# Optimization experiments

Hardware: AMD Instinct MI355X
Metric: run time of the kernel (lower is better)

## Reference

```python
import jax, jax.numpy as jnp
import numpy as np

K, B, D, H, C, T = 3, 512, 1024, 512, 48, 25  # num_TAB, batch, linear_dim, hidden, n_classes, max_len

def setup_inputs() -> dict:
    key = jax.random.key(0)
    ks = jax.random.split(key, 18)
    rn = lambda k, s, sc=0.02: (jax.random.normal(k, s, jnp.float32) * sc)
    return {
        'S_ppps': jax.random.normal(ks[0], (K, B, D), jnp.float32),
        'R_ppps': jax.random.normal(ks[1], (K, B, D), jnp.float32),
        'cls_W': rn(ks[2], (K, 2 * D, C)), 'cls_b': jnp.zeros((K, C), jnp.float32),
        'dur_W': rn(ks[3], (K * D, 1)), 'dur_b': jnp.zeros((1,), jnp.float32),
        'lin_W': rn(ks[4], (2 * K * D + K * C, D + 1)), 'lin_b': jnp.zeros((D + 1,), jnp.float32),
        'W_ih': rn(ks[5], (4 * H, D + 1)), 'W_hh': rn(ks[6], (4 * H, H)),
        'b_ih': jnp.zeros((4 * H,), jnp.float32), 'b_hh': jnp.zeros((4 * H,), jnp.float32),
        'Wp': rn(ks[7], (H, C)), 'bp': jnp.zeros((C,), jnp.float32),
        'Wdur': rn(ks[8], (D + H, 1)), 'bdur': jnp.zeros((1,), jnp.float32),
        'embed': rn(ks[9], (C, D), 1.0),
        'Wattn': rn(ks[10], (H, D)),
    }

def reference(S_ppps, R_ppps, cls_W, cls_b, dur_W, dur_b, lin_W, lin_b,
              W_ih, W_hh, b_ih, b_hh, Wp, bp, Wdur, bdur, embed, Wattn):
    S_stack = jnp.transpose(S_ppps, (1, 0, 2))            # [B,K,D] (torch.stack(S_ppps,1))
    # per-TAB classifiers: Y[i] = softmax(Linear(cat(S_i,R_i)))
    SR = jnp.concatenate([S_ppps, R_ppps], axis=-1)       # [K,B,2D]
    Y = jax.nn.softmax(jnp.einsum('kbd,kdc->kbc', SR, cls_W) + cls_b[:, None, :], axis=-1)  # [K,B,C]
    Yf = jnp.transpose(Y, (1, 0, 2)).reshape(B, K * C)    # cat(Y0..Yk) feature-wise
    Sf = jnp.transpose(S_ppps, (1, 0, 2)).reshape(B, K * D)
    Rf = jnp.transpose(R_ppps, (1, 0, 2)).reshape(B, K * D)
    feat = jnp.concatenate([Yf, Sf, Rf], axis=1)          # [B, K*C + 2*K*D]
    x0 = feat @ lin_W + lin_b                             # [B, D+1]
    curr_dur = Rf @ dur_W + dur_b                         # [B,1]
    inv_sqrt_d = 1.0 / np.sqrt(D).astype(np.float32)

    def step(carry, _):
        x, h, c, prev_h = carry
        gates = x @ W_ih.T + b_ih + h @ W_hh.T + b_hh     # [B,4H], torch gate order i,f,g,o
        i_g, f_g, g_g, o_g = jnp.split(gates, 4, axis=1)
        c = jax.nn.sigmoid(f_g) * c + jax.nn.sigmoid(i_g) * jnp.tanh(g_g)
        h = jax.nn.sigmoid(o_g) * jnp.tanh(c)
        logits = h @ Wp + bp                              # [B,C]
        q = (h @ Wattn) * inv_sqrt_d                      # [B,D]
        aw = jax.nn.softmax(jnp.einsum('bd,bkd->bk', q, S_stack), axis=-1)
        att = jnp.einsum('bk,bkd->bd', aw, S_stack)       # [B,D]
        dur = jnp.concatenate([att, prev_h], axis=1) @ Wdur + bdur  # [B,1]
        labels = jnp.argmax(logits, axis=1)
        probs = jax.nn.softmax(logits, axis=1)
        nx = jnp.concatenate([embed[labels], dur], axis=1)  # [B,D+1]
        return (nx, h, c, h), (labels, probs, dur[:, 0], att)

    z = jnp.zeros((B, H), x0.dtype)
    _, (labels_t, probs_t, dur_t, att_t) = jax.lax.scan(step, (x0, z, z, z), None, length=T)
    curr_action = jnp.sum(Y, axis=0)                      # [B,C]
    pred_class_probs = jnp.transpose(probs_t, (1, 0, 2))  # [B,T,C]
    pred_action_durations = jnp.concatenate([curr_dur, dur_t.T], axis=1)  # [B,T+1]
    return (labels_t, pred_class_probs, curr_action, pred_action_durations, att_t)
```

## Files before the change

kernel.cpp:

```cpp
#include <hip/hip_runtime.h>
#include <math.h>

#define B 512
#define D 1024
#define H 512
#define C 48
#define K 3
#define T 25
#define DP1 1025
#define G4H 2048
#define NC 3120
#define KP 1056
#define FK 6304

typedef _Float16 f16;
typedef _Float16 half8 __attribute__((ext_vector_type(8)));
typedef float floatx4 __attribute__((ext_vector_type(4)));

__device__ __forceinline__ float sigf(float x){ return 1.0f/(1.0f+expf(-x)); }


template<int MODE>
__device__ __forceinline__ void mf_load(
    const f16* __restrict__ Ahi, const f16* __restrict__ Alo,
    const f16* __restrict__ Bhi, const f16* __restrict__ Blo,
    int M, int lda, int ldb, int m0, int n0, int kbase, int k0, int t,
    const f16* __restrict__ Yh, const f16* __restrict__ Yl,
    const float* __restrict__ Sf, const float* __restrict__ Rf,
    half8& rah, half8& ral, half8& rbh, half8& rbl)
{
    int r = t>>2, seg = t&3;
    int kk = k0 + seg*8;
    {
        size_t off = (size_t)(n0+r)*ldb + kbase + kk;
        rbh = *(const half8*)(Bhi + off);
        rbl = *(const half8*)(Blo + off);
    }
    int m = m0 + r;
    if (MODE==0){
        if (m < M){
            size_t off = (size_t)m*lda + kbase + kk;
            rah = *(const half8*)(Ahi + off);
            ral = *(const half8*)(Alo + off);
        } else {
            #pragma unroll
            for (int i=0;i<8;i++){ rah[i]=(f16)0; ral[i]=(f16)0; }
        }
    } else {
        int kabs = kbase + kk;
        if (kabs < 144){
            rah = *(const half8*)(Yh + (size_t)m*144 + kabs);
            ral = *(const half8*)(Yl + (size_t)m*144 + kabs);
        } else if (kabs < 6288){
            int kp = kabs - 144;
            const float* src = (kp < 3*D)
                ? (Sf + (size_t)(kp>>10)*(B*D) + (size_t)m*D + (kp&(D-1)))
                : (Rf + (size_t)((kp-3*D)>>10)*(B*D) + (size_t)m*D + ((kp-3*D)&(D-1)));
            float4 f0 = *(const float4*)src;
            float4 f1 = *(const float4*)(src+4);
            float fv[8]={f0.x,f0.y,f0.z,f0.w,f1.x,f1.y,f1.z,f1.w};
            #pragma unroll
            for (int i=0;i<8;i++){
                f16 h=(f16)fv[i];
                rah[i]=h; ral[i]=(f16)(fv[i]-(float)h);
            }
        } else {
            #pragma unroll
            for (int i=0;i<8;i++){ rah[i]=(f16)0; ral[i]=(f16)0; }
        }
    }
}

template<int MODE>
__global__ __launch_bounds__(256)
void k_mfma(const f16* __restrict__ Ahi, const f16* __restrict__ Alo,
            const f16* __restrict__ Bhi, const f16* __restrict__ Blo,
            float* __restrict__ Cc, const float* __restrict__ bias,
            int M, int Nvalid, int Ktot, int lda, int ldb, int ldc,
            int ksl, size_t cstride, int MB, int Z,
            const f16* __restrict__ Yh, const f16* __restrict__ Yl,
            const float* __restrict__ Sf, const float* __restrict__ Rf)
{
    __shared__ __align__(16) f16 Ash[2][64][40];
    __shared__ __align__(16) f16 Asl[2][64][40];
    __shared__ __align__(16) f16 Bsh[2][64][40];
    __shared__ __align__(16) f16 Bsl[2][64][40];
    int t = threadIdx.x;
    int chunk = gridDim.x >> 3;
    int g = (blockIdx.x & 7)*chunk + (blockIdx.x >> 3);
    int mz   = g % (MB*Z);
    int nblk = g / (MB*Z);
    int mblk = mz / Z;
    int z    = mz % Z;
    int m0 = mblk*64, n0 = nblk*64;
    int kbase = z*ksl;
    int kcnt = (z==Z-1)? (Ktot-kbase) : ksl;
    int nIter = kcnt >> 5;
    int r = t>>2, seg = t&3;
    half8 rah, ral, rbh, rbl;
    mf_load<MODE>(Ahi,Alo,Bhi,Blo,M,lda,ldb,m0,n0,kbase,0,t,Yh,Yl,Sf,Rf,rah,ral,rbh,rbl);
    int lane = t&63, wv = t>>6;
    int lrow = lane&15, quad = lane>>4;
    floatx4 acc[4] = {};
    int cur = 0;
    for (int it=0; it<nIter; ++it){
        *(half8*)&Ash[cur][r][seg*8] = rah;
        *(half8*)&Asl[cur][r][seg*8] = ral;
        *(half8*)&Bsh[cur][r][seg*8] = rbh;
        *(half8*)&Bsl[cur][r][seg*8] = rbl;
        if (it+1 < nIter)
            mf_load<MODE>(Ahi,Alo,Bhi,Blo,M,lda,ldb,m0,n0,kbase,(it+1)<<5,t,Yh,Yl,Sf,Rf,rah,ral,rbh,rbl);
        __syncthreads();
        half8 ah = *(const half8*)&Ash[cur][wv*16+lrow][quad*8];
        half8 al = *(const half8*)&Asl[cur][wv*16+lrow][quad*8];
        #pragma unroll
        for (int j=0;j<4;j++){
            half8 bh = *(const half8*)&Bsh[cur][j*16+lrow][quad*8];
            half8 bl = *(const half8*)&Bsl[cur][j*16+lrow][quad*8];
            acc[j] = __builtin_amdgcn_mfma_f32_16x16x32_f16(ah, bh, acc[j], 0,0,0);
            acc[j] = __builtin_amdgcn_mfma_f32_16x16x32_f16(al, bh, acc[j], 0,0,0);
            acc[j] = __builtin_amdgcn_mfma_f32_16x16x32_f16(ah, bl, acc[j], 0,0,0);
        }
        cur ^= 1;
    }
    float* Cz = Cc + (size_t)z*cstride;
    #pragma unroll
    for (int j=0;j<4;j++){
        int col = n0 + j*16 + lrow;
        if (col >= Nvalid) continue;
        float bv = bias ? bias[col] : 0.f;
        #pragma unroll
        for (int i=0;i<4;i++){
            int row = m0 + wv*16 + quad*4 + i;
            if (row < M) Cz[(size_t)row*ldc + col] = acc[j][i] + bv;
        }
    }
}


__global__ void k_bt_build(const float* __restrict__ src, f16* __restrict__ hi, f16* __restrict__ lo,
                           int Ksrc, int Nsrc, int ld_src, int NB, int KB, float scale){
    __shared__ float tile[32][33];
    int k0 = blockIdx.x*32, n0 = blockIdx.y*32;
    int lx = threadIdx.x & 31, ly = threadIdx.x >> 5;
    for (int rr=0; rr<32; rr+=8){
        int k2 = k0+ly+rr, n = n0+lx;
        tile[ly+rr][lx] = (k2<Ksrc && n<Nsrc)? src[(size_t)k2*ld_src+n]*scale : 0.f;
    }
    __syncthreads();
    for (int rr=0; rr<32; rr+=8){
        int n = n0+ly+rr, k2 = k0+lx;
        if (n<NB && k2<KB){
            float v = tile[lx][ly+rr];
            f16 h=(f16)v;
            hi[(size_t)n*KB+k2]=h;
            lo[(size_t)n*KB+k2]=(f16)(v-(float)h);
        }
    }
}

__global__ void k_permrows(const float* __restrict__ src, f16* __restrict__ hi, f16* __restrict__ lo,
                           int src_ld, int dst_ld, int kvalid){
    int idx = blockIdx.x*256+threadIdx.x;
    if (idx >= G4H*dst_ld) return;
    int p = idx/dst_ld, k2 = idx%dst_ld;
    int j = p>>2, g = p&3, gi = (g<<9)|j;
    float v = (k2<kvalid)? src[(size_t)gi*src_ld + k2] : 0.f;
    f16 h=(f16)v;
    hi[idx]=h; lo[idx]=(f16)(v-(float)h);
}

__global__ void k_cvt(const float* __restrict__ src, f16* __restrict__ hi, f16* __restrict__ lo,
                      int M, int ld_src, int nvalid, int ld_dst){
    int idx = blockIdx.x*256+threadIdx.x;
    if (idx >= M*ld_dst) return;
    int m = idx/ld_dst, n = idx%ld_dst;
    float v = (n<nvalid)? src[(size_t)m*ld_src+n] : 0.f;
    f16 h=(f16)v; hi[idx]=h; lo[idx]=(f16)(v-(float)h);
}

__global__ void k_cvtY(const float* __restrict__ Y, f16* __restrict__ hi, f16* __restrict__ lo){
    int idx = blockIdx.x*256+threadIdx.x;
    if (idx >= B*144) return;
    int b = idx/144, k2 = idx%144;
    float v = Y[((size_t)(k2/C)*B + b)*C + (k2%C)];
    f16 h=(f16)v; hi[idx]=h; lo[idx]=(f16)(v-(float)h);
}

__global__ void k_zeroh(f16* a, f16* b2, int n){
    int i = blockIdx.x*256+threadIdx.x; if (i<n){ a[i]=(f16)0; b2[i]=(f16)0; }
}

__global__ void k_prep(const float* __restrict__ bih, const float* __restrict__ bhh,
                       const float* __restrict__ bp, const float* __restrict__ Wih,
                       float* __restrict__ bias2p, float* __restrict__ biascat,
                       float* __restrict__ wl){
    int i = blockIdx.x*256 + threadIdx.x;
    if (i < G4H){
        int g=i&3, j=i>>2; int gi=(g<<9)|j;
        bias2p[i]=bih[gi]+bhh[gi];
        wl[i]=Wih[(size_t)gi*DP1 + 1024];
    }
    if (i < C) biascat[i]=bp[i];
}

__global__ void k_cls(const float* __restrict__ S, const float* __restrict__ R,
                      const float* __restrict__ clsW, const float* __restrict__ clsb,
                      float* __restrict__ Y){
    int kb = blockIdx.x; int k = kb / B; int b = kb % B;
    int t = threadIdx.x;
    __shared__ float sr[64];
    __shared__ float lg[C];
    __shared__ float mred[2];
    float acc = (t<C) ? clsb[k*C+t] : 0.f;
    const float* W = clsW + (size_t)k*2*D*C;
    for (int i0=0; i0<2*D; i0+=64){
        int i = i0 + t;
        sr[t] = (i < D) ? S[((size_t)k*B+b)*D + i] : R[((size_t)k*B+b)*D + (i-D)];
        __syncthreads();
        if (t < C){ for (int ii=0; ii<64; ++ii) acc += sr[ii]*W[(size_t)(i0+ii)*C + t]; }
        __syncthreads();
    }
    if (t<C) lg[t]=acc;
    __syncthreads();
    if (t==0){
        float m=lg[0]; for(int c2=1;c2<C;c2++) m=fmaxf(m,lg[c2]);
        float s=0.f; for(int c2=0;c2<C;c2++) s+=expf(lg[c2]-m);
        mred[0]=m; mred[1]=s;
    }
    __syncthreads();
    if (t<C) Y[((size_t)k*B+b)*C + t] = expf(lg[t]-mred[0])/mred[1];
}

__global__ void k_curr_action(const float* __restrict__ Y, float* __restrict__ outca){
    int i = blockIdx.x*256+threadIdx.x; if (i>=B*C) return;
    int b=i/C, c2=i%C;
    outca[i] = Y[((size_t)0*B+b)*C+c2] + Y[((size_t)1*B+b)*C+c2] + Y[((size_t)2*B+b)*C+c2];
}

__global__ void k_dur0(const float* __restrict__ R, const float* __restrict__ durW,
                       const float* __restrict__ durb, float* __restrict__ outpad){
    int b = blockIdx.x; int t = threadIdx.x;
    __shared__ float red[256];
    float p=0.f;
    for (int i=t; i<K*D; i+=256){ int k=i>>10, d=i&1023; p += R[((size_t)k*B+b)*D+d]*durW[i]; }
    red[t]=p; __syncthreads();
    for (int s=128;s>0;s>>=1){ if(t<s) red[t]+=red[t+s]; __syncthreads(); }
    if (t==0) outpad[(size_t)b*(T+1)] = red[0] + durb[0];
}

__global__ void k_red(float* __restrict__ dst, const float* __restrict__ src, int parts, size_t pstride,
                      int M, int Nld, int Nvalid, const float* __restrict__ bias){
    int idx = blockIdx.x*256+threadIdx.x;
    if (idx >= M*Nld) return;
    int n = idx % Nld;
    float v = 0.f;
    if (n < Nvalid){
        for (int p=0;p<parts;p++) v += src[(size_t)p*pstride + idx];
        if (bias) v += bias[n];
    }
    dst[idx]=v;
}

__global__ void k_redcvt(const float* __restrict__ src, int parts, size_t pstride,
                         const float* __restrict__ bias, f16* __restrict__ hi, f16* __restrict__ lo){
    int idx = blockIdx.x*256+threadIdx.x;
    if (idx >= 512*KP) return;
    int m = idx/KP, n = idx%KP;
    float v = 0.f;
    if (n < DP1){
        for (int p=0;p<parts;p++) v += src[(size_t)p*pstride + (size_t)m*1028 + n];
        v += bias[n];
    }
    f16 h=(f16)v; hi[idx]=h; lo[idx]=(f16)(v-(float)h);
}


__global__ void k_lstm0(const float* __restrict__ gxp, int parts, size_t pstride,
                        const float* __restrict__ bias2p,
                        float* __restrict__ c, f16* __restrict__ hhi, f16* __restrict__ hlo){
    int idx = blockIdx.x*256+threadIdx.x; if (idx>=B*H) return;
    int r=idx>>9, j=idx&511;
    float4 g = *(const float4*)&gxp[(size_t)r*G4H + (j<<2)];
    if (parts==2){
        float4 g2 = *(const float4*)&gxp[pstride + (size_t)r*G4H + (j<<2)];
        g.x+=g2.x; g.y+=g2.y; g.z+=g2.z; g.w+=g2.w;
    }
    float4 bb = *(const float4*)&bias2p[j<<2];
    g.x+=bb.x; g.y+=bb.y; g.z+=bb.z; g.w+=bb.w;
    float cn = sigf(g.x)*tanhf(g.z);
    c[idx]=cn;
    float hv = sigf(g.w)*tanhf(cn);
    f16 h=(f16)hv; hhi[idx]=h; hlo[idx]=(f16)(hv-(float)h);
}

__global__ void k_postapply(const float* __restrict__ rawg, int parts, size_t pstride,
                       const float* __restrict__ S,
                       const f16* __restrict__ holdhi, const f16* __restrict__ holdlo,
                       const float* __restrict__ E, const float* __restrict__ wl,
                       const float* __restrict__ biascat,
                       const float* __restrict__ Wdur, const float* __restrict__ bdur,
                       float* __restrict__ outlab, float* __restrict__ outprobs,
                       float* __restrict__ outatt, float* __restrict__ outpad,
                       int* __restrict__ labs, float* __restrict__ wsdur,
                       float* __restrict__ c, f16* __restrict__ hNhi, f16* __restrict__ hNlo,
                       int tstep, int doLstm)
{
    int b=blockIdx.x, t=threadIdx.x;
    int lane=t&63, wv=t>>6;
    __shared__ float lg[C];
    __shared__ float aw[3];
    __shared__ float redw[4][8];
    __shared__ int sbest;
    __shared__ float sdv;
    const float* z0 = rawg + (size_t)b*NC;
    const float* z1 = z0 + pstride;
    if (t<C){
        float v = z0[G4H+t]; if (parts==2) v += z1[G4H+t];
        lg[t] = v + biascat[t];
    }
    if (t<64){
        float m = (t<C)? lg[t] : -1e30f;
        int bi = t;
        #pragma unroll
        for (int s=32;s>0;s>>=1){
            float om=__shfl_down(m,s); int ob=__shfl_down(bi,s);
            if (om>m || (om==m && ob<bi)){ m=om; bi=ob; }
        }
        m=__shfl(m,0); bi=__shfl(bi,0);
        float e=(t<C)? expf(lg[t]-m):0.f;
        float ss=e;
        #pragma unroll
        for (int s=32;s>0;s>>=1) ss+=__shfl_down(ss,s);
        ss=__shfl(ss,0);
        if (t==0){
            labs[b]=bi; sbest=bi;
            outlab[(size_t)tstep*B+b]=(float)bi;
        }
        if (t<C) outprobs[(size_t)b*(T*C)+tstep*C+t]=expf(lg[t]-m)/ss;
    }
    const float* S0 = S + (size_t)b*D;
    const float* S1 = S0 + (size_t)B*D;
    const float* S2 = S1 + (size_t)B*D;
    const float* q0 = z0 + G4H + C;
    const float* q1 = z1 + G4H + C;
    float pv0=0.f,pv1=0.f,pv2=0.f;
    for (int d=t; d<D; d+=512){
        float qd=q0[d]; if (parts==2) qd+=q1[d];
        pv0+=qd*S0[d]; pv1+=qd*S1[d]; pv2+=qd*S2[d];
    }
    #pragma unroll
    for (int s=32;s>0;s>>=1){
        pv0+=__shfl_down(pv0,s); pv1+=__shfl_down(pv1,s); pv2+=__shfl_down(pv2,s);
    }
    if (lane==0){ redw[0][wv]=pv0; redw[1][wv]=pv1; redw[2][wv]=pv2; }
    __syncthreads();
    if (t==0){
        float a0=0.f,a1=0.f,a2=0.f;
        #pragma unroll
        for (int w=0;w<8;w++){ a0+=redw[0][w]; a1+=redw[1][w]; a2+=redw[2][w]; }
        float m=fmaxf(a0,fmaxf(a1,a2));
        float e0=expf(a0-m), e1=expf(a1-m), e2=expf(a2-m);
        float si=1.f/(e0+e1+e2);
        aw[0]=e0*si; aw[1]=e1*si; aw[2]=e2*si;
    }
    __syncthreads();
    float a0=aw[0],a1=aw[1],a2=aw[2];
    float dp=0.f;
    for (int d=t; d<D; d+=512){
        float av=a0*S0[d]+a1*S1[d]+a2*S2[d];
        outatt[(size_t)tstep*B*D + (size_t)b*D + d]=av;
        dp+=av*Wdur[d];
    }
    if (holdhi){
        for (int p=t;p<H;p+=512)
            dp += ((float)holdhi[(size_t)b*H+p] + (float)holdlo[(size_t)b*H+p])*Wdur[D+p];
    }
    #pragma unroll
    for (int s=32;s>0;s>>=1) dp+=__shfl_down(dp,s);
    if (lane==0) redw[3][wv]=dp;
    __syncthreads();
    if (t==0){
        float dv=0.f;
        #pragma unroll
        for (int w=0;w<8;w++) dv+=redw[3][w];
        dv += bdur[0];
        outpad[(size_t)b*(T+1)+tstep+1]=dv; wsdur[b]=dv; sdv=dv;
    }
    __syncthreads();
    if (doLstm){
        int lb=sbest; float dv=sdv;
        int j=t;
        float4 g4 = *(const float4*)&z0[4*j];
        if (parts==2){
            float4 h4 = *(const float4*)&z1[4*j];
            g4.x+=h4.x; g4.y+=h4.y; g4.z+=h4.z; g4.w+=h4.w;
        }
        float4 e4 = *(const float4*)&E[(size_t)lb*G4H+4*j];
        float4 w4 = *(const float4*)&wl[4*j];
        float gi=g4.x+e4.x+dv*w4.x;
        float gf=g4.y+e4.y+dv*w4.y;
        float gg=g4.z+e4.z+dv*w4.z;
        float go=g4.w+e4.w+dv*w4.w;
        size_t ci=(size_t)b*H+j;
        float cn = sigf(gf)*c[ci] + sigf(gi)*tanhf(gg);
        c[ci]=cn;
        float hv = sigf(go)*tanhf(cn);
        f16 hh=(f16)hv;
        hNhi[ci]=hh; hNlo[ci]=(f16)(hv-(float)hh);
    }
}


extern "C" void kernel_launch(void* const* d_in, const int* in_sizes, int n_in,
                              void* d_out, int out_size, void* d_ws, size_t ws_size,
                              hipStream_t stream) {
    const float* S    = (const float*)d_in[0];
    const float* R    = (const float*)d_in[1];
    const float* clsW = (const float*)d_in[2];
    const float* clsb = (const float*)d_in[3];
    const float* durW = (const float*)d_in[4];
    const float* durb = (const float*)d_in[5];
    const float* linW = (const float*)d_in[6];
    const float* linb = (const float*)d_in[7];
    const float* Wih  = (const float*)d_in[8];
    const float* Whh  = (const float*)d_in[9];
    const float* bih  = (const float*)d_in[10];
    const float* bhh  = (const float*)d_in[11];
    const float* Wp   = (const float*)d_in[12];
    const float* bp   = (const float*)d_in[13];
    const float* Wdur = (const float*)d_in[14];
    const float* bdur = (const float*)d_in[15];
    const float* embed= (const float*)d_in[16];
    const float* Wattn= (const float*)d_in[17];

    float* out = (float*)d_out;
    float* outlab   = out;
    float* outprobs = out + 12800;
    float* outca    = out + 627200;
    float* outpad   = out + 651776;
    float* outatt   = out + 665088;

    float* ws = (float*)d_ws;
    float* E       = ws + 0;
    float* wl      = ws + 98304;
    float* bias2p  = ws + 100352;
    float* biascat = ws + 102400;
    float* c       = ws + 102464;
    f16*   hAhi    = (f16*)(ws + 364608);
    f16*   hAlo    = (f16*)(ws + 495680);
    f16*   hBhi    = (f16*)(ws + 626752);
    f16*   hBlo    = (f16*)(ws + 757824);
    float* wsdur   = ws + 888896;
    int*   labs    = (int*)(ws + 889408);
    f16*   Yhi     = (f16*)(ws + 889920);
    f16*   Ylo     = (f16*)(ws + 926784);
    float* Y       = ws + 963648;
    f16*   x0hi    = (f16*)(ws + 1563712);
    f16*   x0lo    = (f16*)(ws + 1834048);
    f16*   embhi   = (f16*)(ws + 2104384);
    f16*   emblo   = (f16*)(ws + 2129728);
    const size_t SB = 2155072;
    f16*   lwthi   = (f16*)(ws + SB);
    f16*   lwtlo   = (f16*)(ws + SB + 3429376);
    float* x0part  = ws + SB + 6858752;
    f16*   Wcthi   = (f16*)(ws + SB);
    f16*   Wctlo   = (f16*)(ws + SB + 802816);
    f16*   Wihphi  = (f16*)(ws + SB + 1605632);
    f16*   Wihplo  = (f16*)(ws + SB + 2686976);
    float* rawg    = ws + SB + 4816896;
    float* gpart   = rawg;

    int ZX0, ksl_x0;
    if      (ws_size >= (size_t)52898048){ ZX0=8; ksl_x0=800;  }
    else if (ws_size >= (size_t)44476672){ ZX0=4; ksl_x0=1600; }
    else                                 { ZX0=2; ksl_x0=3168; }
    int ZSC    = (ws_size >= (size_t)40667392) ? 2 : 1;
    int ksl_sc = (ZSC==2) ? 256 : 512;
    const int ZGX = 2, ksl_gx = 544;
    const int ZE  = 4, ksl_e  = 256;

    k_prep<<<8,256,0,stream>>>(bih,bhh,bp,Wih,bias2p,biascat,wl);
    k_cls<<<K*B,64,0,stream>>>(S,R,clsW,clsb,Y);
    k_curr_action<<<(B*C+255)/256,256,0,stream>>>(Y,outca);
    k_cvtY<<<(B*144+255)/256,256,0,stream>>>(Y,Yhi,Ylo);
    k_dur0<<<B,256,0,stream>>>(R,durW,durb,outpad);
    k_bt_build<<<dim3((FK+31)/32,(1088+31)/32),256,0,stream>>>(linW,lwthi,lwtlo,6288,1025,1025,1088,FK,1.f);
    k_mfma<1><<<8*17*ZX0,256,0,stream>>>(nullptr,nullptr,lwthi,lwtlo,x0part,nullptr,
                                         512,1028,FK,0,FK,1028,ksl_x0,(size_t)512*1028,8,ZX0,
                                         Yhi,Ylo,S,R);
    k_redcvt<<<(512*KP+255)/256,256,0,stream>>>(x0part,ZX0,(size_t)512*1028,linb,x0hi,x0lo);
    k_permrows<<<(G4H*KP+255)/256,256,0,stream>>>(Wih,Wihphi,Wihplo,DP1,KP,DP1);
    k_mfma<0><<<8*32*ZGX,256,0,stream>>>(x0hi,x0lo,Wihphi,Wihplo,gpart,nullptr,
                                         512,G4H,KP,KP,KP,G4H,ksl_gx,(size_t)512*G4H,8,ZGX,
                                         nullptr,nullptr,nullptr,nullptr);
    k_lstm0<<<(B*H+255)/256,256,0,stream>>>(gpart,ZGX,(size_t)512*G4H,bias2p,c,hAhi,hAlo);
    k_cvt<<<(48*KP+255)/256,256,0,stream>>>(embed,embhi,emblo,48,1024,1024,KP);
    k_mfma<0><<<1*32*ZE,256,0,stream>>>(embhi,emblo,Wihphi,Wihplo,gpart,nullptr,
                                        48,G4H,KP,KP,KP,G4H,ksl_e,(size_t)48*G4H,1,ZE,
                                        nullptr,nullptr,nullptr,nullptr);
    k_red<<<(48*G4H+255)/256,256,0,stream>>>(E,gpart,ZE,(size_t)48*G4H,48,G4H,G4H,bias2p);
    k_permrows<<<(G4H*512+255)/256,256,0,stream>>>(Whh,Wcthi,Wctlo,H,H,H);
    k_bt_build<<<dim3(16,2),256,0,stream>>>(Wp,Wcthi+(size_t)2048*512,Wctlo+(size_t)2048*512,
                                            512,48,48,48,512,1.f);
    k_bt_build<<<dim3(16,32),256,0,stream>>>(Wattn,Wcthi+(size_t)2096*512,Wctlo+(size_t)2096*512,
                                             512,1024,1024,1024,512,0.03125f);
    k_zeroh<<<32,256,0,stream>>>(Wcthi+(size_t)3120*512,Wctlo+(size_t)3120*512,16*512);

    size_t pstr = (size_t)512*NC;
    f16 *hCurHi=hAhi, *hCurLo=hAlo, *hPrvHi=hBhi, *hPrvLo=hBlo;
    for (int t=0;t<T;t++){
        k_mfma<0><<<8*49*ZSC,256,0,stream>>>(hCurHi,hCurLo,Wcthi,Wctlo,rawg,nullptr,
                                             512,NC,H,H,H,NC,ksl_sc,pstr,8,ZSC,
                                             nullptr,nullptr,nullptr,nullptr);
        k_postapply<<<B,512,0,stream>>>(rawg,ZSC,pstr,S,(t==0)?nullptr:hPrvHi,(t==0)?nullptr:hPrvLo,
                                        E,wl,biascat,Wdur,bdur,
                                        outlab,outprobs,outatt,outpad,labs,wsdur,
                                        c,hPrvHi,hPrvLo,t,(t<T-1)?1:0);
        f16* th=hPrvHi; hPrvHi=hCurHi; hCurHi=th;
        f16* tl=hPrvLo; hPrvLo=hCurLo; hCurLo=tl;
    }
}
```

Baseline: 972.0 us.

## Fuse LSTM scan into persistent kernel with grid-wide atomic barriers

Replaces the per-timestep pair of GEMM and postprocessing launches with a single persistent kernel that loops over all timesteps and synchronises blocks through an atomic counter barrier. The recurrent weight high-part tile is kept resident in LDS, and cell and previous hidden state stay in registers. Each wave handles one batch row in the postprocessing phase. This removes launch overhead and split-K partial buffers, but relies on all 196 blocks being co-resident and adds spin-barrier cost per step.

```diff
diff --git a/kernel.cpp b/kernel.cpp
--- a/kernel.cpp
+++ b/kernel.cpp
@@ -12,6 +12,7 @@
 #define NC 3120
 #define KP 1056
 #define FK 6304
+#define NBLK 196
 
 typedef _Float16 f16;
 typedef _Float16 half8 __attribute__((ext_vector_type(8)));
@@ -194,8 +195,9 @@
 __global__ void k_prep(const float* __restrict__ bih, const float* __restrict__ bhh,
                        const float* __restrict__ bp, const float* __restrict__ Wih,
                        float* __restrict__ bias2p, float* __restrict__ biascat,
-                       float* __restrict__ wl){
+                       float* __restrict__ wl, unsigned* __restrict__ bar){
     int i = blockIdx.x*256 + threadIdx.x;
+    if (i == 0) *bar = 0u;
     if (i < G4H){
         int g=i&3, j=i>>2; int gi=(g<<9)|j;
         bias2p[i]=bih[gi]+bhh[gi];
@@ -275,7 +277,6 @@
     f16 h=(f16)v; hi[idx]=h; lo[idx]=(f16)(v-(float)h);
 }
 
-
 __global__ void k_lstm0(const float* __restrict__ gxp, int parts, size_t pstride,
                         const float* __restrict__ bias2p,
                         float* __restrict__ c, f16* __restrict__ hhi, f16* __restrict__ hlo){
@@ -294,120 +295,222 @@
     f16 h=(f16)hv; hhi[idx]=h; hlo[idx]=(f16)(hv-(float)h);
 }
 
-__global__ void k_postapply(const float* __restrict__ rawg, int parts, size_t pstride,
-                       const float* __restrict__ S,
-                       const f16* __restrict__ holdhi, const f16* __restrict__ holdlo,
-                       const float* __restrict__ E, const float* __restrict__ wl,
-                       const float* __restrict__ biascat,
-                       const float* __restrict__ Wdur, const float* __restrict__ bdur,
-                       float* __restrict__ outlab, float* __restrict__ outprobs,
-                       float* __restrict__ outatt, float* __restrict__ outpad,
-                       int* __restrict__ labs, float* __restrict__ wsdur,
-                       float* __restrict__ c, f16* __restrict__ hNhi, f16* __restrict__ hNlo,
-                       int tstep, int doLstm)
+__global__ __launch_bounds__(256,1)
+void k_scan(const f16* __restrict__ Bh_g, const f16* __restrict__ Bl_g,
+            f16* __restrict__ ghhi, f16* __restrict__ ghlo,
+            const float* __restrict__ cinit,
+            float* __restrict__ rawg,
+            const float* __restrict__ S,
+            const float* __restrict__ E, const float* __restrict__ wl,
+            const float* __restrict__ biascat,
+            const float* __restrict__ Wdur, const float* __restrict__ bdur,
+            float* __restrict__ outlab, float* __restrict__ outprobs,
+            float* __restrict__ outatt, float* __restrict__ outpad,
+            unsigned* __restrict__ bar)
 {
-    int b=blockIdx.x, t=threadIdx.x;
-    int lane=t&63, wv=t>>6;
-    __shared__ float lg[C];
-    __shared__ float aw[3];
-    __shared__ float redw[4][8];
-    __shared__ int sbest;
-    __shared__ float sdv;
-    const float* z0 = rawg + (size_t)b*NC;
-    const float* z1 = z0 + pstride;
-    if (t<C){
-        float v = z0[G4H+t]; if (parts==2) v += z1[G4H+t];
-        lg[t] = v + biascat[t];
-    }
-    if (t<64){
-        float m = (t<C)? lg[t] : -1e30f;
-        int bi = t;
+    __shared__ __align__(16) f16 Bsh[64][520];
+    __shared__ __align__(16) f16 Ash[2][128][40];
+    __shared__ __align__(16) f16 Asl[2][128][40];
+    const int t = threadIdx.x;
+    const int g = blockIdx.x;
+    const int lane = t & 63, wv = t >> 6;
+    const int lrow = lane & 15, quad = lane >> 4;
+    const int mblk = g & 3, nblk = g >> 2;
+    const int m0 = mblk << 7, n0 = nblk << 6;
+
+    for (int q = t; q < 64*64; q += 256){
+        int col = q >> 6, seg = q & 63;
+        *(half8*)&Bsh[col][seg<<3] = *(const half8*)(Bh_g + (size_t)(n0+col)*H + (seg<<3));
+    }
+
+    const int brow = g + NBLK*wv;
+    const bool act = brow < B;
+    float c_reg[8], hold_reg[8], hcur_reg[8];
+    if (act){
         #pragma unroll
-        for (int s=32;s>0;s>>=1){
-            float om=__shfl_down(m,s); int ob=__shfl_down(bi,s);
-            if (om>m || (om==m && ob<bi)){ m=om; bi=ob; }
-        }
-        m=__shfl(m,0); bi=__shfl(bi,0);
-        float e=(t<C)? expf(lg[t]-m):0.f;
-        float ss=e;
+        for (int i=0;i<8;i++){
+            int j = lane + (i<<6);
+            c_reg[i]   = cinit[(size_t)brow*H + j];
+            hold_reg[i]= 0.f;
+            hcur_reg[i]= (float)ghhi[(size_t)brow*H + j] + (float)ghlo[(size_t)brow*H + j];
+        }
+    }
+    const float bd0 = bdur[0];
+    unsigned gp = 0;
+    __syncthreads();
+
+    for (int ts=0; ts<T; ++ts){
+        floatx4 acc[2][4] = {};
+        half8 pa0h,pa0l,pa1h,pa1l;
+        {
+            int r0 = t>>2, s0 = (t&3)<<3;
+            size_t o0 = (size_t)(m0+r0)*H + s0;
+            size_t o1 = (size_t)(m0+64+r0)*H + s0;
+            pa0h = *(const half8*)(ghhi+o0); pa0l = *(const half8*)(ghlo+o0);
+            pa1h = *(const half8*)(ghhi+o1); pa1l = *(const half8*)(ghlo+o1);
+        }
+        half8 bl[2][4];
         #pragma unroll
-        for (int s=32;s>0;s>>=1) ss+=__shfl_down(ss,s);
-        ss=__shfl(ss,0);
+        for (int j=0;j<4;j++)
+            bl[0][j] = *(const half8*)(Bl_g + (size_t)(n0+j*16+lrow)*H + (quad<<3));
+        #pragma unroll 4
+        for (int it=0; it<16; ++it){
+            const int cur = it & 1;
+            *(half8*)&Ash[cur][t>>2][(t&3)<<3]        = pa0h;
+            *(half8*)&Asl[cur][t>>2][(t&3)<<3]        = pa0l;
+            *(half8*)&Ash[cur][64+(t>>2)][(t&3)<<3]   = pa1h;
+            *(half8*)&Asl[cur][64+(t>>2)][(t&3)<<3]   = pa1l;
+            if (it+1<16){
+                int r0 = t>>2, s0 = (t&3)<<3;
+                size_t o0 = (size_t)(m0+r0)*H + (it+1)*32 + s0;
+                size_t o1 = (size_t)(m0+64+r0)*H + (it+1)*32 + s0;
+                pa0h = *(const half8*)(ghhi+o0); pa0l = *(const half8*)(ghlo+o0);
+                pa1h = *(const half8*)(ghhi+o1); pa1l = *(const half8*)(ghlo+o1);
+            }
+            asm volatile("s_waitcnt lgkmcnt(0)" ::: "memory");
+            __builtin_amdgcn_s_barrier();
+            if (it+1<16){
+                #pragma unroll
+                for (int j=0;j<4;j++)
+                    bl[(it+1)&1][j] = *(const half8*)(Bl_g + (size_t)(n0+j*16+lrow)*H + (it+1)*32 + (quad<<3));
+            }
+            half8 ah0 = *(const half8*)&Ash[cur][(wv<<5)+lrow][quad<<3];
+            half8 al0 = *(const half8*)&Asl[cur][(wv<<5)+lrow][quad<<3];
+            half8 ah1 = *(const half8*)&Ash[cur][(wv<<5)+16+lrow][quad<<3];
+            half8 al1 = *(const half8*)&Asl[cur][(wv<<5)+16+lrow][quad<<3];
+            #pragma unroll
+            for (int j=0;j<4;j++){
+                half8 bh  = *(const half8*)&Bsh[j*16+lrow][(it<<5)+(quad<<3)];
+                half8 blj = bl[cur][j];
+                acc[0][j] = __builtin_amdgcn_mfma_f32_16x16x32_f16(ah0,bh, acc[0][j],0,0,0);
+                acc[0][j] = __builtin_amdgcn_mfma_f32_16x16x32_f16(al0,bh, acc[0][j],0,0,0);
+                acc[0][j] = __builtin_amdgcn_mfma_f32_16x16x32_f16(ah0,blj,acc[0][j],0,0,0);
+                acc[1][j] = __builtin_amdgcn_mfma_f32_16x16x32_f16(ah1,bh, acc[1][j],0,0,0);
+                acc[1][j] = __builtin_amdgcn_mfma_f32_16x16x32_f16(al1,bh, acc[1][j],0,0,0);
+                acc[1][j] = __builtin_amdgcn_mfma_f32_16x16x32_f16(ah1,blj,acc[1][j],0,0,0);
+            }
+        }
+        #pragma unroll
+        for (int j=0;j<4;j++){
+            int col = n0 + j*16 + lrow;
+            if (col < NC){
+                #pragma unroll
+                for (int rt=0;rt<2;rt++){
+                    int rbase = m0 + (wv<<5) + rt*16 + (quad<<2);
+                    #pragma unroll
+                    for (int i=0;i<4;i++)
+                        rawg[(size_t)(rbase+i)*NC + col] = acc[rt][j][i];
+                }
+            }
+        }
+        ++gp;
+        __syncthreads();
         if (t==0){
-            labs[b]=bi; sbest=bi;
-            outlab[(size_t)tstep*B+b]=(float)bi;
-        }
-        if (t<C) outprobs[(size_t)b*(T*C)+tstep*C+t]=expf(lg[t]-m)/ss;
-    }
-    const float* S0 = S + (size_t)b*D;
-    const float* S1 = S0 + (size_t)B*D;
-    const float* S2 = S1 + (size_t)B*D;
-    const float* q0 = z0 + G4H + C;
-    const float* q1 = z1 + G4H + C;
-    float pv0=0.f,pv1=0.f,pv2=0.f;
-    for (int d=t; d<D; d+=512){
-        float qd=q0[d]; if (parts==2) qd+=q1[d];
-        pv0+=qd*S0[d]; pv1+=qd*S1[d]; pv2+=qd*S2[d];
-    }
-    #pragma unroll
-    for (int s=32;s>0;s>>=1){
-        pv0+=__shfl_down(pv0,s); pv1+=__shfl_down(pv1,s); pv2+=__shfl_down(pv2,s);
-    }
-    if (lane==0){ redw[0][wv]=pv0; redw[1][wv]=pv1; redw[2][wv]=pv2; }
-    __syncthreads();
-    if (t==0){
-        float a0=0.f,a1=0.f,a2=0.f;
-        #pragma unroll
-        for (int w=0;w<8;w++){ a0+=redw[0][w]; a1+=redw[1][w]; a2+=redw[2][w]; }
-        float m=fmaxf(a0,fmaxf(a1,a2));
-        float e0=expf(a0-m), e1=expf(a1-m), e2=expf(a2-m);
-        float si=1.f/(e0+e1+e2);
-        aw[0]=e0*si; aw[1]=e1*si; aw[2]=e2*si;
-    }
-    __syncthreads();
-    float a0=aw[0],a1=aw[1],a2=aw[2];
-    float dp=0.f;
-    for (int d=t; d<D; d+=512){
-        float av=a0*S0[d]+a1*S1[d]+a2*S2[d];
-        outatt[(size_t)tstep*B*D + (size_t)b*D + d]=av;
-        dp+=av*Wdur[d];
-    }
-    if (holdhi){
-        for (int p=t;p<H;p+=512)
-            dp += ((float)holdhi[(size_t)b*H+p] + (float)holdlo[(size_t)b*H+p])*Wdur[D+p];
-    }
-    #pragma unroll
-    for (int s=32;s>0;s>>=1) dp+=__shfl_down(dp,s);
-    if (lane==0) redw[3][wv]=dp;
-    __syncthreads();
-    if (t==0){
-        float dv=0.f;
-        #pragma unroll
-        for (int w=0;w<8;w++) dv+=redw[3][w];
-        dv += bdur[0];
-        outpad[(size_t)b*(T+1)+tstep+1]=dv; wsdur[b]=dv; sdv=dv;
-    }
-    __syncthreads();
-    if (doLstm){
-        int lb=sbest; float dv=sdv;
-        int j=t;
-        float4 g4 = *(const float4*)&z0[4*j];
-        if (parts==2){
-            float4 h4 = *(const float4*)&z1[4*j];
-            g4.x+=h4.x; g4.y+=h4.y; g4.z+=h4.z; g4.w+=h4.w;
-        }
-        float4 e4 = *(const float4*)&E[(size_t)lb*G4H+4*j];
-        float4 w4 = *(const float4*)&wl[4*j];
-        float gi=g4.x+e4.x+dv*w4.x;
-        float gf=g4.y+e4.y+dv*w4.y;
-        float gg=g4.z+e4.z+dv*w4.z;
-        float go=g4.w+e4.w+dv*w4.w;
-        size_t ci=(size_t)b*H+j;
-        float cn = sigf(gf)*c[ci] + sigf(gi)*tanhf(gg);
-        c[ci]=cn;
-        float hv = sigf(go)*tanhf(cn);
-        f16 hh=(f16)hv;
-        hNhi[ci]=hh; hNlo[ci]=(f16)(hv-(float)hh);
+            __threadfence();
+            __hip_atomic_fetch_add(bar, 1u, __ATOMIC_RELEASE, __HIP_MEMORY_SCOPE_AGENT);
+            while (__hip_atomic_load(bar, __ATOMIC_ACQUIRE, __HIP_MEMORY_SCOPE_AGENT) < gp*NBLK)
+                __builtin_amdgcn_s_sleep(1);
+            __threadfence();
+        }
+        __syncthreads();
+
+        if (act){
+            const float* z0 = rawg + (size_t)brow*NC;
+            float lgv = (lane<C)? (z0[G4H+lane] + biascat[lane]) : -3.0e38f;
+            float mx = lgv; int bi = lane;
+            #pragma unroll
+            for (int s2=32;s2>0;s2>>=1){
+                float om = __shfl_xor(mx, s2); int ob = __shfl_xor(bi, s2);
+                if (om>mx || (om==mx && ob<bi)){ mx=om; bi=ob; }
+            }
+            float ev = (lane<C)? expf(lgv-mx) : 0.f;
+            float ss = ev;
+            #pragma unroll
+            for (int s2=32;s2>0;s2>>=1) ss += __shfl_xor(ss, s2);
+            if (lane<C) outprobs[(size_t)brow*(T*C) + ts*C + lane] = ev/ss;
+            if (lane==0) outlab[(size_t)ts*B + brow] = (float)bi;
+            const float* S0  = S + (size_t)brow*D;
+            const float* S1  = S0 + (size_t)B*D;
+            const float* S2p = S1 + (size_t)B*D;
+            const float* q   = z0 + G4H + C;
+            float p0=0.f,p1=0.f,p2=0.f;
+            #pragma unroll
+            for (int i=0;i<4;i++){
+                int d = ((i<<6)+lane)<<2;
+                float4 qv = *(const float4*)(q+d);
+                float4 s0 = *(const float4*)(S0+d);
+                float4 s1 = *(const float4*)(S1+d);
+                float4 s2 = *(const float4*)(S2p+d);
+                p0 += qv.x*s0.x+qv.y*s0.y+qv.z*s0.z+qv.w*s0.w;
+                p1 += qv.x*s1.x+qv.y*s1.y+qv.z*s1.z+qv.w*s1.w;
+                p2 += qv.x*s2.x+qv.y*s2.y+qv.z*s2.z+qv.w*s2.w;
+            }
+            #pragma unroll
+            for (int s2=32;s2>0;s2>>=1){
+                p0 += __shfl_xor(p0,s2); p1 += __shfl_xor(p1,s2); p2 += __shfl_xor(p2,s2);
+            }
+            float mm = fmaxf(p0,fmaxf(p1,p2));
+            float e0 = expf(p0-mm), e1 = expf(p1-mm), e2 = expf(p2-mm);
+            float inv = 1.f/(e0+e1+e2);
+            float a0=e0*inv, a1=e1*inv, a2=e2*inv;
+            float dp = 0.f;
+            float* attp = outatt + (size_t)ts*B*D + (size_t)brow*D;
+            #pragma unroll
+            for (int i=0;i<4;i++){
+                int d = ((i<<6)+lane)<<2;
+                float4 s0 = *(const float4*)(S0+d);
+                float4 s1 = *(const float4*)(S1+d);
+                float4 s2 = *(const float4*)(S2p+d);
+                float4 w4 = *(const float4*)(Wdur+d);
+                float4 av;
+                av.x = a0*s0.x+a1*s1.x+a2*s2.x;
+                av.y = a0*s0.y+a1*s1.y+a2*s2.y;
+                av.z = a0*s0.z+a1*s1.z+a2*s2.z;
+                av.w = a0*s0.w+a1*s1.w+a2*s2.w;
+                *(float4*)(attp+d) = av;
+                dp += av.x*w4.x+av.y*w4.y+av.z*w4.z+av.w*w4.w;
+            }
+            #pragma unroll
+            for (int i=0;i<8;i++) dp += hold_reg[i]*Wdur[D + lane + (i<<6)];
+            #pragma unroll
+            for (int s2=32;s2>0;s2>>=1) dp += __shfl_xor(dp,s2);
+            float dv = dp + bd0;
+            if (lane==0) outpad[(size_t)brow*(T+1) + ts + 1] = dv;
+            if (ts < T-1){
+                const float* Erow = E + (size_t)bi*G4H;
+                #pragma unroll
+                for (int i=0;i<8;i++){
+                    int j = lane + (i<<6);
+                    float4 g4 = *(const float4*)(z0 + (j<<2));
+                    float4 e4 = *(const float4*)(Erow + (j<<2));
+                    float4 w4 = *(const float4*)(wl + (j<<2));
+                    float gi = g4.x+e4.x+dv*w4.x;
+                    float gf = g4.y+e4.y+dv*w4.y;
+                    float gg = g4.z+e4.z+dv*w4.z;
+                    float go = g4.w+e4.w+dv*w4.w;
+                    float cn = sigf(gf)*c_reg[i] + sigf(gi)*tanhf(gg);
+                    c_reg[i] = cn;
+                    float hv = sigf(go)*tanhf(cn);
+                    f16 hh = (f16)hv;
+                    ghhi[(size_t)brow*H + j] = hh;
+                    ghlo[(size_t)brow*H + j] = (f16)(hv-(float)hh);
+                    hold_reg[i] = hcur_reg[i];
+                    hcur_reg[i] = hv;
+                }
+            }
+        }
+        if (ts+1 < T){
+            ++gp;
+            __syncthreads();
+            if (t==0){
+                __threadfence();
+                __hip_atomic_fetch_add(bar, 1u, __ATOMIC_RELEASE, __HIP_MEMORY_SCOPE_AGENT);
+                while (__hip_atomic_load(bar, __ATOMIC_ACQUIRE, __HIP_MEMORY_SCOPE_AGENT) < gp*NBLK)
+                    __builtin_amdgcn_s_sleep(1);
+                __threadfence();
+            }
+            __syncthreads();
+        }
     }
 }
 
@@ -449,10 +552,7 @@
     float* c       = ws + 102464;
     f16*   hAhi    = (f16*)(ws + 364608);
     f16*   hAlo    = (f16*)(ws + 495680);
-    f16*   hBhi    = (f16*)(ws + 626752);
-    f16*   hBlo    = (f16*)(ws + 757824);
-    float* wsdur   = ws + 888896;
-    int*   labs    = (int*)(ws + 889408);
+    unsigned* bar  = (unsigned*)(ws + 889408);
     f16*   Yhi     = (f16*)(ws + 889920);
     f16*   Ylo     = (f16*)(ws + 926784);
     float* Y       = ws + 963648;
@@ -475,12 +575,10 @@
     if      (ws_size >= (size_t)52898048){ ZX0=8; ksl_x0=800;  }
     else if (ws_size >= (size_t)44476672){ ZX0=4; ksl_x0=1600; }
     else                                 { ZX0=2; ksl_x0=3168; }
-    int ZSC    = (ws_size >= (size_t)40667392) ? 2 : 1;
-    int ksl_sc = (ZSC==2) ? 256 : 512;
     const int ZGX = 2, ksl_gx = 544;
     const int ZE  = 4, ksl_e  = 256;
 
-    k_prep<<<8,256,0,stream>>>(bih,bhh,bp,Wih,bias2p,biascat,wl);
+    k_prep<<<8,256,0,stream>>>(bih,bhh,bp,Wih,bias2p,biascat,wl,bar);
     k_cls<<<K*B,64,0,stream>>>(S,R,clsW,clsb,Y);
     k_curr_action<<<(B*C+255)/256,256,0,stream>>>(Y,outca);
     k_cvtY<<<(B*144+255)/256,256,0,stream>>>(Y,Yhi,Ylo);
@@ -507,17 +605,6 @@
                                              512,1024,1024,1024,512,0.03125f);
     k_zeroh<<<32,256,0,stream>>>(Wcthi+(size_t)3120*512,Wctlo+(size_t)3120*512,16*512);
 
-    size_t pstr = (size_t)512*NC;
-    f16 *hCurHi=hAhi, *hCurLo=hAlo, *hPrvHi=hBhi, *hPrvLo=hBlo;
-    for (int t=0;t<T;t++){
-        k_mfma<0><<<8*49*ZSC,256,0,stream>>>(hCurHi,hCurLo,Wcthi,Wctlo,rawg,nullptr,
-                                             512,NC,H,H,H,NC,ksl_sc,pstr,8,ZSC,
-                                             nullptr,nullptr,nullptr,nullptr);
-        k_postapply<<<B,512,0,stream>>>(rawg,ZSC,pstr,S,(t==0)?nullptr:hPrvHi,(t==0)?nullptr:hPrvLo,
-                                        E,wl,biascat,Wdur,bdur,
-                                        outlab,outprobs,outatt,outpad,labs,wsdur,
-                                        c,hPrvHi,hPrvLo,t,(t<T-1)?1:0);
-        f16* th=hPrvHi; hPrvHi=hCurHi; hCurHi=th;
-        f16* tl=hPrvLo; hPrvLo=hCurLo; hCurLo=tl;
-    }
-}
+    k_scan<<<NBLK,256,0,stream>>>(Wcthi,Wctlo,hAhi,hAlo,c,rawg,S,E,wl,biascat,Wdur,bdur,
+                                  outlab,outprobs,outatt,outpad,bar);
+}
```

Result: slower. 2.044 ms (+110.3%).

## Precompute S·Wattnᵀ so attention scores use hidden state directly

Applied to the files above, without the earlier changes.

Uses associativity: q·S_k = h·(Wattn·S_kᵀ), so V = S·Wattnᵀ (scaled) is computed once before the loop with an MFMA GEMM. The per-step GEMM then drops the 1024 attention-query columns (NC from 3120 to 2112), and the attention scores become a 512-wide dot of h with V inside the post kernel. The post kernel is also tidied with xor-shuffles, vectorized float2 loads, and unused label and duration workspace writes removed. The trade-off is an extra setup GEMM plus conversions and a change in rounding order for the scores.

```diff
diff --git a/kernel.cpp b/kernel.cpp
--- a/kernel.cpp
+++ b/kernel.cpp
@@ -9,7 +9,8 @@
 #define T 25
 #define DP1 1025
 #define G4H 2048
-#define NC 3120
+#define NC 2112
+#define NCV 2096
 #define KP 1056
 #define FK 6304
 
@@ -77,7 +78,7 @@
             const f16* __restrict__ Bhi, const f16* __restrict__ Blo,
             float* __restrict__ Cc, const float* __restrict__ bias,
             int M, int Nvalid, int Ktot, int lda, int ldb, int ldc,
-            int ksl, size_t cstride, int MB, int Z,
+            int ksl, size_t cstride, int MB, int Z, int zmaj,
             const f16* __restrict__ Yh, const f16* __restrict__ Yl,
             const float* __restrict__ Sf, const float* __restrict__ Rf)
 {
@@ -86,12 +87,19 @@
     __shared__ __align__(16) f16 Bsh[2][64][40];
     __shared__ __align__(16) f16 Bsl[2][64][40];
     int t = threadIdx.x;
-    int chunk = gridDim.x >> 3;
-    int g = (blockIdx.x & 7)*chunk + (blockIdx.x >> 3);
-    int mz   = g % (MB*Z);
-    int nblk = g / (MB*Z);
-    int mblk = mz / Z;
-    int z    = mz % Z;
+    int mblk, nblk, z;
+    if (zmaj){
+        z = blockIdx.x % Z;
+        int rest = blockIdx.x / Z;
+        mblk = rest % MB; nblk = rest / MB;
+    } else {
+        int chunk = gridDim.x >> 3;
+        int g = (blockIdx.x & 7)*chunk + (blockIdx.x >> 3);
+        int mz = g % (MB*Z);
+        nblk = g / (MB*Z);
+        mblk = mz / Z;
+        z    = mz % Z;
+    }
     int m0 = mblk*64, n0 = nblk*64;
     int kbase = z*ksl;
     int kcnt = (z==Z-1)? (Ktot-kbase) : ksl;
@@ -171,11 +179,11 @@
 }
 
 __global__ void k_cvt(const float* __restrict__ src, f16* __restrict__ hi, f16* __restrict__ lo,
-                      int M, int ld_src, int nvalid, int ld_dst){
+                      int M, int ld_src, int nvalid, int ld_dst, float scale){
     int idx = blockIdx.x*256+threadIdx.x;
     if (idx >= M*ld_dst) return;
     int m = idx/ld_dst, n = idx%ld_dst;
-    float v = (n<nvalid)? src[(size_t)m*ld_src+n] : 0.f;
+    float v = (n<nvalid)? src[(size_t)m*ld_src+n]*scale : 0.f;
     f16 h=(f16)v; hi[idx]=h; lo[idx]=(f16)(v-(float)h);
 }
 
@@ -295,65 +303,56 @@
 }
 
 __global__ void k_postapply(const float* __restrict__ rawg, int parts, size_t pstride,
-                       const float* __restrict__ S,
+                       const float* __restrict__ S, const float* __restrict__ V,
+                       const f16* __restrict__ hchi, const f16* __restrict__ hclo,
                        const f16* __restrict__ holdhi, const f16* __restrict__ holdlo,
                        const float* __restrict__ E, const float* __restrict__ wl,
                        const float* __restrict__ biascat,
                        const float* __restrict__ Wdur, const float* __restrict__ bdur,
                        float* __restrict__ outlab, float* __restrict__ outprobs,
                        float* __restrict__ outatt, float* __restrict__ outpad,
-                       int* __restrict__ labs, float* __restrict__ wsdur,
                        float* __restrict__ c, f16* __restrict__ hNhi, f16* __restrict__ hNlo,
                        int tstep, int doLstm)
 {
     int b=blockIdx.x, t=threadIdx.x;
     int lane=t&63, wv=t>>6;
-    __shared__ float lg[C];
     __shared__ float aw[3];
     __shared__ float redw[4][8];
     __shared__ int sbest;
     __shared__ float sdv;
     const float* z0 = rawg + (size_t)b*NC;
     const float* z1 = z0 + pstride;
-    if (t<C){
-        float v = z0[G4H+t]; if (parts==2) v += z1[G4H+t];
-        lg[t] = v + biascat[t];
-    }
     if (t<64){
-        float m = (t<C)? lg[t] : -1e30f;
-        int bi = t;
+        float lgv = -3.0e38f;
+        if (t<C){
+            float v = z0[G4H+t]; if (parts==2) v += z1[G4H+t];
+            lgv = v + biascat[t];
+        }
+        float m = lgv; int bi = t;
         #pragma unroll
-        for (int s=32;s>0;s>>=1){
-            float om=__shfl_down(m,s); int ob=__shfl_down(bi,s);
+        for (int s2=32;s2>0;s2>>=1){
+            float om=__shfl_xor(m,s2); int ob=__shfl_xor(bi,s2);
             if (om>m || (om==m && ob<bi)){ m=om; bi=ob; }
         }
-        m=__shfl(m,0); bi=__shfl(bi,0);
-        float e=(t<C)? expf(lg[t]-m):0.f;
+        float e=(t<C)? expf(lgv-m):0.f;
         float ss=e;
         #pragma unroll
-        for (int s=32;s>0;s>>=1) ss+=__shfl_down(ss,s);
-        ss=__shfl(ss,0);
+        for (int s2=32;s2>0;s2>>=1) ss+=__shfl_xor(ss,s2);
+        if (t<C) outprobs[(size_t)b*(T*C)+tstep*C+t]=e/ss;
         if (t==0){
-            labs[b]=bi; sbest=bi;
+            sbest=bi;
             outlab[(size_t)tstep*B+b]=(float)bi;
         }
-        if (t<C) outprobs[(size_t)b*(T*C)+tstep*C+t]=expf(lg[t]-m)/ss;
-    }
-    const float* S0 = S + (size_t)b*D;
-    const float* S1 = S0 + (size_t)B*D;
-    const float* S2 = S1 + (size_t)B*D;
-    const float* q0 = z0 + G4H + C;
-    const float* q1 = z1 + G4H + C;
-    float pv0=0.f,pv1=0.f,pv2=0.f;
-    for (int d=t; d<D; d+=512){
-        float qd=q0[d]; if (parts==2) qd+=q1[d];
-        pv0+=qd*S0[d]; pv1+=qd*S1[d]; pv2+=qd*S2[d];
-    }
+    }
+    float hv_t = (float)hchi[(size_t)b*H + t] + (float)hclo[(size_t)b*H + t];
+    float p0 = hv_t * V[((size_t)(0*B+b))*H + t];
+    float p1 = hv_t * V[((size_t)(1*B+b))*H + t];
+    float p2 = hv_t * V[((size_t)(2*B+b))*H + t];
     #pragma unroll
-    for (int s=32;s>0;s>>=1){
-        pv0+=__shfl_down(pv0,s); pv1+=__shfl_down(pv1,s); pv2+=__shfl_down(pv2,s);
-    }
-    if (lane==0){ redw[0][wv]=pv0; redw[1][wv]=pv1; redw[2][wv]=pv2; }
+    for (int s2=32;s2>0;s2>>=1){
+        p0 += __shfl_xor(p0,s2); p1 += __shfl_xor(p1,s2); p2 += __shfl_xor(p2,s2);
+    }
+    if (lane==0){ redw[0][wv]=p0; redw[1][wv]=p1; redw[2][wv]=p2; }
     __syncthreads();
     if (t==0){
         float a0=0.f,a1=0.f,a2=0.f;
@@ -366,18 +365,29 @@
     }
     __syncthreads();
     float a0=aw[0],a1=aw[1],a2=aw[2];
-    float dp=0.f;
-    for (int d=t; d<D; d+=512){
-        float av=a0*S0[d]+a1*S1[d]+a2*S2[d];
-        outatt[(size_t)tstep*B*D + (size_t)b*D + d]=av;
-        dp+=av*Wdur[d];
+    const float* S0  = S + (size_t)b*D;
+    const float* S1  = S0 + (size_t)B*D;
+    const float* S2p = S1 + (size_t)B*D;
+    float dp = 0.f;
+    float* attp = outatt + (size_t)tstep*B*D + (size_t)b*D;
+    {
+        int d = t<<1;
+        float2 s0 = *(const float2*)(S0+d);
+        float2 s1 = *(const float2*)(S1+d);
+        float2 s2 = *(const float2*)(S2p+d);
+        float2 w2 = *(const float2*)(Wdur+d);
+        float2 av;
+        av.x = a0*s0.x+a1*s1.x+a2*s2.x;
+        av.y = a0*s0.y+a1*s1.y+a2*s2.y;
+        *(float2*)(attp+d) = av;
+        dp += av.x*w2.x+av.y*w2.y;
     }
     if (holdhi){
-        for (int p=t;p<H;p+=512)
-            dp += ((float)holdhi[(size_t)b*H+p] + (float)holdlo[(size_t)b*H+p])*Wdur[D+p];
+        float hvo = (float)holdhi[(size_t)b*H+t] + (float)holdlo[(size_t)b*H+t];
+        dp += hvo * Wdur[D+t];
     }
     #pragma unroll
-    for (int s=32;s>0;s>>=1) dp+=__shfl_down(dp,s);
+    for (int s2=32;s2>0;s2>>=1) dp += __shfl_xor(dp,s2);
     if (lane==0) redw[3][wv]=dp;
     __syncthreads();
     if (t==0){
@@ -385,7 +395,7 @@
         #pragma unroll
         for (int w=0;w<8;w++) dv+=redw[3][w];
         dv += bdur[0];
-        outpad[(size_t)b*(T+1)+tstep+1]=dv; wsdur[b]=dv; sdv=dv;
+        outpad[(size_t)b*(T+1)+tstep+1]=dv; sdv=dv;
     }
     __syncthreads();
     if (doLstm){
@@ -398,10 +408,10 @@
         }
         float4 e4 = *(const float4*)&E[(size_t)lb*G4H+4*j];
         float4 w4 = *(const float4*)&wl[4*j];
-        float gi=g4.x+e4.x+dv*w4.x;
-        float gf=g4.y+e4.y+dv*w4.y;
-        float gg=g4.z+e4.z+dv*w4.z;
-        float go=g4.w+e4.w+dv*w4.w;
+        float gi = g4.x+e4.x+dv*w4.x;
+        float gf = g4.y+e4.y+dv*w4.y;
+        float gg = g4.z+e4.z+dv*w4.z;
+        float go = g4.w+e4.w+dv*w4.w;
         size_t ci=(size_t)b*H+j;
         float cn = sigf(gf)*c[ci] + sigf(gi)*tanhf(gg);
         c[ci]=cn;
@@ -451,11 +461,11 @@
     f16*   hAlo    = (f16*)(ws + 495680);
     f16*   hBhi    = (f16*)(ws + 626752);
     f16*   hBlo    = (f16*)(ws + 757824);
-    float* wsdur   = ws + 888896;
-    int*   labs    = (int*)(ws + 889408);
     f16*   Yhi     = (f16*)(ws + 889920);
     f16*   Ylo     = (f16*)(ws + 926784);
     float* Y       = ws + 963648;
+    f16*   watthi  = (f16*)(ws + 1037376);
+    f16*   wattlo  = (f16*)(ws + 1299520);
     f16*   x0hi    = (f16*)(ws + 1563712);
     f16*   x0lo    = (f16*)(ws + 1834048);
     f16*   embhi   = (f16*)(ws + 2104384);
@@ -465,20 +475,22 @@
     f16*   lwtlo   = (f16*)(ws + SB + 3429376);
     float* x0part  = ws + SB + 6858752;
     f16*   Wcthi   = (f16*)(ws + SB);
-    f16*   Wctlo   = (f16*)(ws + SB + 802816);
-    f16*   Wihphi  = (f16*)(ws + SB + 1605632);
-    f16*   Wihplo  = (f16*)(ws + SB + 2686976);
-    float* rawg    = ws + SB + 4816896;
+    f16*   Wctlo   = (f16*)(ws + SB + 540672);
+    f16*   Wihphi  = (f16*)(ws + SB + 1081344);
+    f16*   Wihplo  = (f16*)(ws + SB + 2162688);
+    f16*   Shi     = (f16*)(ws + SB + 3244032);
+    f16*   Slo     = (f16*)(ws + SB + 4030464);
+    float* Vbuf    = ws + SB + 4816896;
+    float* rawg    = ws + SB + 5603328;
     float* gpart   = rawg;
 
     int ZX0, ksl_x0;
     if      (ws_size >= (size_t)52898048){ ZX0=8; ksl_x0=800;  }
     else if (ws_size >= (size_t)44476672){ ZX0=4; ksl_x0=1600; }
     else                                 { ZX0=2; ksl_x0=3168; }
-    int ZSC    = (ws_size >= (size_t)40667392) ? 2 : 1;
-    int ksl_sc = (ZSC==2) ? 256 : 512;
     const int ZGX = 2, ksl_gx = 544;
     const int ZE  = 4, ksl_e  = 256;
+    const int ZSC = 2, ksl_sc = 256;
 
     k_prep<<<8,256,0,stream>>>(bih,bhh,bp,Wih,bias2p,biascat,wl);
     k_cls<<<K*B,64,0,stream>>>(S,R,clsW,clsb,Y);
@@ -487,35 +499,39 @@
     k_dur0<<<B,256,0,stream>>>(R,durW,durb,outpad);
     k_bt_build<<<dim3((FK+31)/32,(1088+31)/32),256,0,stream>>>(linW,lwthi,lwtlo,6288,1025,1025,1088,FK,1.f);
     k_mfma<1><<<8*17*ZX0,256,0,stream>>>(nullptr,nullptr,lwthi,lwtlo,x0part,nullptr,
-                                         512,1028,FK,0,FK,1028,ksl_x0,(size_t)512*1028,8,ZX0,
+                                         512,1028,FK,0,FK,1028,ksl_x0,(size_t)512*1028,8,ZX0,1,
                                          Yhi,Ylo,S,R);
     k_redcvt<<<(512*KP+255)/256,256,0,stream>>>(x0part,ZX0,(size_t)512*1028,linb,x0hi,x0lo);
     k_permrows<<<(G4H*KP+255)/256,256,0,stream>>>(Wih,Wihphi,Wihplo,DP1,KP,DP1);
     k_mfma<0><<<8*32*ZGX,256,0,stream>>>(x0hi,x0lo,Wihphi,Wihplo,gpart,nullptr,
-                                         512,G4H,KP,KP,KP,G4H,ksl_gx,(size_t)512*G4H,8,ZGX,
+                                         512,G4H,KP,KP,KP,G4H,ksl_gx,(size_t)512*G4H,8,ZGX,0,
                                          nullptr,nullptr,nullptr,nullptr);
     k_lstm0<<<(B*H+255)/256,256,0,stream>>>(gpart,ZGX,(size_t)512*G4H,bias2p,c,hAhi,hAlo);
-    k_cvt<<<(48*KP+255)/256,256,0,stream>>>(embed,embhi,emblo,48,1024,1024,KP);
+    k_cvt<<<(48*KP+255)/256,256,0,stream>>>(embed,embhi,emblo,48,1024,1024,KP,1.f);
     k_mfma<0><<<1*32*ZE,256,0,stream>>>(embhi,emblo,Wihphi,Wihplo,gpart,nullptr,
-                                        48,G4H,KP,KP,KP,G4H,ksl_e,(size_t)48*G4H,1,ZE,
+                                        48,G4H,KP,KP,KP,G4H,ksl_e,(size_t)48*G4H,1,ZE,0,
                                         nullptr,nullptr,nullptr,nullptr);
     k_red<<<(48*G4H+255)/256,256,0,stream>>>(E,gpart,ZE,(size_t)48*G4H,48,G4H,G4H,bias2p);
+    k_cvt<<<(1536*1024+255)/256,256,0,stream>>>(S,Shi,Slo,1536,1024,1024,1024,1.f);
+    k_cvt<<<(512*1024+255)/256,256,0,stream>>>(Wattn,watthi,wattlo,512,1024,1024,1024,0.03125f);
+    k_mfma<0><<<24*8,256,0,stream>>>(Shi,Slo,watthi,wattlo,Vbuf,nullptr,
+                                     1536,512,1024,1024,1024,512,1024,0,24,1,0,
+                                     nullptr,nullptr,nullptr,nullptr);
     k_permrows<<<(G4H*512+255)/256,256,0,stream>>>(Whh,Wcthi,Wctlo,H,H,H);
     k_bt_build<<<dim3(16,2),256,0,stream>>>(Wp,Wcthi+(size_t)2048*512,Wctlo+(size_t)2048*512,
                                             512,48,48,48,512,1.f);
-    k_bt_build<<<dim3(16,32),256,0,stream>>>(Wattn,Wcthi+(size_t)2096*512,Wctlo+(size_t)2096*512,
-                                             512,1024,1024,1024,512,0.03125f);
-    k_zeroh<<<32,256,0,stream>>>(Wcthi+(size_t)3120*512,Wctlo+(size_t)3120*512,16*512);
+    k_zeroh<<<32,256,0,stream>>>(Wcthi+(size_t)2096*512,Wctlo+(size_t)2096*512,16*512);
 
     size_t pstr = (size_t)512*NC;
     f16 *hCurHi=hAhi, *hCurLo=hAlo, *hPrvHi=hBhi, *hPrvLo=hBlo;
     for (int t=0;t<T;t++){
-        k_mfma<0><<<8*49*ZSC,256,0,stream>>>(hCurHi,hCurLo,Wcthi,Wctlo,rawg,nullptr,
-                                             512,NC,H,H,H,NC,ksl_sc,pstr,8,ZSC,
+        k_mfma<0><<<8*33*ZSC,256,0,stream>>>(hCurHi,hCurLo,Wcthi,Wctlo,rawg,nullptr,
+                                             512,NCV,H,H,H,NC,ksl_sc,pstr,8,ZSC,0,
                                              nullptr,nullptr,nullptr,nullptr);
-        k_postapply<<<B,512,0,stream>>>(rawg,ZSC,pstr,S,(t==0)?nullptr:hPrvHi,(t==0)?nullptr:hPrvLo,
+        k_postapply<<<B,512,0,stream>>>(rawg,ZSC,pstr,S,Vbuf,hCurHi,hCurLo,
+                                        (t==0)?nullptr:hPrvHi,(t==0)?nullptr:hPrvLo,
                                         E,wl,biascat,Wdur,bdur,
-                                        outlab,outprobs,outatt,outpad,labs,wsdur,
+                                        outlab,outprobs,outatt,outpad,
                                         c,hPrvHi,hPrvLo,t,(t<T-1)?1:0);
         f16* th=hPrvHi; hPrvHi=hCurHi; hCurHi=th;
         f16* tl=hPrvLo; hPrvLo=hCurLo; hCurLo=tl;
```

Measured after the change: 910.2 us. 1.07x faster.
